# Kernel optimization log

Measured on AMD Instinct MI355X. Metric: run time of the kernel, lower is better.

## Reference

```python
import jax, jax.numpy as jnp
import numpy as np

HIDDEN_DIM = 256
Z_DIM = 64
B = 8
SRC_LEN = 2048
NUM_DIRS = 2


def setup_inputs() -> dict:
    key = jax.random.key(0)
    ks = jax.random.split(key, 7)
    return {
        "encoder_hidden_state": jax.random.normal(ks[0], (NUM_DIRS, B, HIDDEN_DIM), dtype=jnp.float32),
        "decoder_hidden_state": jax.random.normal(ks[1], (B, HIDDEN_DIM), dtype=jnp.float32),
        "latent_z_seq": jax.random.normal(ks[2], (B, SRC_LEN, Z_DIM), dtype=jnp.float32),
        "mask": jax.random.randint(ks[3], (B, SRC_LEN), 0, 2, dtype=jnp.int32),
        "weight_q": jax.random.normal(ks[4], (HIDDEN_DIM + Z_DIM, HIDDEN_DIM), dtype=jnp.float32),
        "weight_k": jax.random.normal(ks[5], (HIDDEN_DIM + Z_DIM, HIDDEN_DIM), dtype=jnp.float32),
        "weight_v": jax.random.normal(ks[6], (HIDDEN_DIM + Z_DIM, HIDDEN_DIM), dtype=jnp.float32),
    }


def reference(encoder_hidden_state, decoder_hidden_state, latent_z_seq, mask,
              weight_q, weight_k, weight_v):
    # decoder_hidden_state is accepted but unused (as in the original forward).
    src_len = latent_z_seq.shape[1]
    temperature = jnp.asarray(HIDDEN_DIM ** 0.5, latent_z_seq.dtype)
    # sum over directions/layers: [D,B,H] -> [B,H], broadcast along seq
    enc = jnp.sum(encoder_hidden_state, axis=0)  # [B,H]
    enc = jnp.broadcast_to(enc[:, None, :], (enc.shape[0], src_len, enc.shape[1]))
    attn_input = jnp.concatenate((enc, latent_z_seq), axis=2)  # [B,S,H+Z]
    q = jnp.einsum('bsd,dh->bsh', attn_input, weight_q)
    k = jnp.einsum('bsd,dh->bsh', attn_input, weight_k)
    v = jnp.einsum('bsd,dh->bsh', attn_input, weight_v)
    scores = jnp.einsum('bqh,bkh->bqk', q, k) / temperature  # [B,S,S]
    # mask[:, :, None] broadcasts along the key axis (masks query rows)
    scores = jnp.where(mask[:, :, None] == 0, jnp.asarray(-1e9, scores.dtype), scores)
    attn = jax.nn.softmax(scores, axis=-1)
    output = jnp.einsum('bqk,bkh->bqh', attn, v)  # [B,S,H]
    return (output, attn)
```

## Files before the change

### kernel.cpp

```cpp
#include <hip/hip_runtime.h>
#include <hip/hip_bf16.h>

#define B_ 8
#define S_ 2048
#define H_ 256
#define Z_ 64
#define CHK 32
#define NQCH 16
#define BS (B_*S_)
#define PSLD 40

typedef short bf16x8 __attribute__((ext_vector_type(8)));
typedef float f32x4 __attribute__((ext_vector_type(4)));

__device__ __forceinline__ unsigned short f2bf(float f) {
  __hip_bfloat16 h = __float2bfloat16(f);
  return *reinterpret_cast<unsigned short*>(&h);
}
__device__ __forceinline__ float bf2f(unsigned short u) {
  __hip_bfloat16 h;
  *reinterpret_cast<unsigned short*>(&h) = u;
  return __bfloat162float(h);
}

__device__ __forceinline__ void gl_lds16(const void* g, void* l) {
  __builtin_amdgcn_global_load_lds(
      (const __attribute__((address_space(1))) unsigned int*)(uintptr_t)g,
      (__attribute__((address_space(3))) unsigned int*)(uintptr_t)l,
      16, 0, 0);
}

__global__ __launch_bounds__(256) void k0_base(
    const float* __restrict__ enc, const float* __restrict__ Wq,
    const float* __restrict__ Wk, const float* __restrict__ Wv,
    float* __restrict__ q0, float* __restrict__ k0, float* __restrict__ v0) {
  int b = blockIdx.x;
  int h = threadIdx.x;
  __shared__ float encs[H_];
  encs[h] = enc[b*H_ + h] + enc[B_*H_ + b*H_ + h];
  __syncthreads();
  float aq = 0.f, ak = 0.f, av = 0.f;
  #pragma unroll 4
  for (int d = 0; d < H_; d++) {
    float e = encs[d];
    aq = fmaf(e, Wq[d*H_ + h], aq);
    ak = fmaf(e, Wk[d*H_ + h], ak);
    av = fmaf(e, Wv[d*H_ + h], av);
  }
  q0[b*H_ + h] = aq;
  k0[b*H_ + h] = ak;
  v0[b*H_ + h] = av;
}

__global__ __launch_bounds__(256) void k1_prep(
    const float* __restrict__ z, const float* __restrict__ Wq,
    const float* __restrict__ Wk, const float* __restrict__ Wv,
    const float* __restrict__ q0, const float* __restrict__ k0b, const float* __restrict__ v0,
    unsigned short* __restrict__ Qhi, unsigned short* __restrict__ Qlo,
    unsigned short* __restrict__ Khi, unsigned short* __restrict__ Klo,
    unsigned short* __restrict__ Vt) {
  int b  = blockIdx.x >> 7;
  int st = blockIdx.x & 127;
  int tid = threadIdx.x;
  __shared__ float zs[16*Z_];
  __shared__ float vbuf[16][H_];
  {
    const float4* zp = reinterpret_cast<const float4*>(z + ((size_t)b*S_ + st*16)*Z_);
    reinterpret_cast<float4*>(zs)[tid] = zp[tid];
  }
  __syncthreads();
  float bq = q0[b*H_ + tid], bk = k0b[b*H_ + tid], bv = v0[b*H_ + tid];
  float accq[16], acck[16], accv[16];
  #pragma unroll
  for (int s = 0; s < 16; s++) { accq[s] = bq; acck[s] = bk; accv[s] = bv; }
  #pragma unroll 2
  for (int z0 = 0; z0 < Z_; z0 += 8) {
    float wq[8], wk[8], wv[8];
    #pragma unroll
    for (int j = 0; j < 8; j++) {
      wq[j] = Wq[(H_+z0+j)*H_ + tid];
      wk[j] = Wk[(H_+z0+j)*H_ + tid];
      wv[j] = Wv[(H_+z0+j)*H_ + tid];
    }
    #pragma unroll
    for (int j = 0; j < 8; j++) {
      #pragma unroll
      for (int s = 0; s < 16; s++) {
        float zz = zs[s*Z_ + z0 + j];
        accq[s] = fmaf(zz, wq[j], accq[s]);
        acck[s] = fmaf(zz, wk[j], acck[s]);
        accv[s] = fmaf(zz, wv[j], accv[s]);
      }
    }
  }
  #pragma unroll
  for (int s = 0; s < 16; s++) {
    size_t row = ((size_t)b*S_ + st*16 + s)*H_ + tid;
    unsigned short qh = f2bf(accq[s]);
    Qhi[row] = qh;
    Qlo[row] = f2bf(accq[s] - bf2f(qh));
    unsigned short kh = f2bf(acck[s]);
    Khi[row] = kh;
    Klo[row] = f2bf(acck[s] - bf2f(kh));
    vbuf[s][tid] = accv[s];
  }
  __syncthreads();
  unsigned int pk[8];
  #pragma unroll
  for (int j = 0; j < 8; j++) {
    pk[j] = (unsigned int)f2bf(vbuf[2*j][tid]) |
            ((unsigned int)f2bf(vbuf[2*j+1][tid]) << 16);
  }
  uint4* vt4 = reinterpret_cast<uint4*>(Vt + ((size_t)b*H_ + tid)*S_ + st*16);
  vt4[0] = make_uint4(pk[0], pk[1], pk[2], pk[3]);
  vt4[1] = make_uint4(pk[4], pk[5], pk[6], pk[7]);
}

__global__ __launch_bounds__(256, 1) void k2_flash(
    const unsigned short* __restrict__ Qhi, const unsigned short* __restrict__ Qlo,
    const unsigned short* __restrict__ Khi, const unsigned short* __restrict__ Klo,
    const unsigned short* __restrict__ Vt, const int* __restrict__ mask,
    float* __restrict__ attn, float* __restrict__ Mq,
    unsigned short* __restrict__ Opart) {
  int bb    = blockIdx.x;
  int b     = bb & 7;
  int strip = (bb >> 3) & 15;
  int kq    = bb >> 7;
  int qb    = strip*128;
  int k0q   = kq*512;
  int tid  = threadIdx.x;
  int wave = tid >> 6;
  int lane = tid & 63;
  int l15  = lane & 15;
  int quad = lane >> 4;
  int qw   = qb + wave*32;

  __shared__ __align__(16) unsigned short KhiL[2][32*256];
  __shared__ __align__(16) unsigned short KloL[2][32*256];
  __shared__ __align__(16) unsigned short VtL[2][256*32];
  __shared__ __align__(16) unsigned short Ps[4][2][16*PSLD];

  const unsigned short* KhiB = Khi + (size_t)b*S_*H_;
  const unsigned short* KloB = Klo + (size_t)b*S_*H_;
  const unsigned short* VtB  = Vt  + (size_t)b*H_*S_;

  int sub = lane >> 5;
  int c5  = lane & 31;
  int hl  = lane >> 2;
  int jj  = lane & 3;

  auto dma_chunk = [&](int c) {
    int buf = c & 1;
    int kc = k0q + c*CHK;
    #pragma unroll
    for (int t = 0; t < 4; t++) {
      int i = wave*4 + t;
      int row = i*2 + sub;
      size_t gs = (size_t)(kc + row)*H_ + ((c5 ^ row)*8);
      gl_lds16(KhiB + gs, &KhiL[buf][i*512]);
      gl_lds16(KloB + gs, &KloL[buf][i*512]);
    }
    #pragma unroll
    for (int t = 0; t < 4; t++) {
      int i = wave*4 + t;
      int h = i*16 + hl;
      gl_lds16(VtB + (size_t)h*S_ + kc + ((jj ^ (hl & 3))*8), &VtL[buf][i*512]);
    }
  };

  bf16x8 qh[2][8], ql[2][8];
  #pragma unroll
  for (int qt = 0; qt < 2; qt++) {
    const unsigned short* qhp = Qhi + ((size_t)b*S_ + qw + qt*16 + l15)*H_ + quad*8;
    const unsigned short* qlp = Qlo + ((size_t)b*S_ + qw + qt*16 + l15)*H_ + quad*8;
    #pragma unroll
    for (int dc = 0; dc < 8; dc++) {
      qh[qt][dc] = *reinterpret_cast<const bf16x8*>(qhp + dc*32);
      ql[qt][dc] = *reinterpret_cast<const bf16x8*>(qlp + dc*32);
    }
  }
  int mrow[2][4];
  #pragma unroll
  for (int qt = 0; qt < 2; qt++)
    #pragma unroll
    for (int r = 0; r < 4; r++) mrow[qt][r] = mask[b*S_ + qw + qt*16 + quad*4 + r];

  f32x4 acc_o[2][16];
  #pragma unroll
  for (int qt = 0; qt < 2; qt++)
    #pragma unroll
    for (int ht = 0; ht < 16; ht++) acc_o[qt][ht] = (f32x4){0.f, 0.f, 0.f, 0.f};
  float m_run[2][4] = {{-1e30f,-1e30f,-1e30f,-1e30f},{-1e30f,-1e30f,-1e30f,-1e30f}};

  dma_chunk(0);
  __syncthreads();

  for (int c = 0; c < NQCH; c++) {
    if (c+1 < NQCH) dma_chunk(c+1);
    int buf = c & 1;
    int kc  = k0q + c*CHK;
    f32x4 sacc[2][2];
    #pragma unroll
    for (int kt = 0; kt < 2; kt++) {
      int row = kt*16 + l15;
      const unsigned short* khb = &KhiL[buf][row*256];
      const unsigned short* klb = &KloL[buf][row*256];
      f32x4 a0[2], a1[2];
      #pragma unroll
      for (int qt = 0; qt < 2; qt++) {
        a0[qt] = (f32x4){0.f,0.f,0.f,0.f};
        a1[qt] = (f32x4){0.f,0.f,0.f,0.f};
      }
      #pragma unroll
      for (int dc = 0; dc < 8; dc += 2) {
        int s0 = ((dc*4 + quad) ^ row) * 8;
        int s1 = (((dc+1)*4 + quad) ^ row) * 8;
        bf16x8 kh0 = *reinterpret_cast<const bf16x8*>(khb + s0);
        bf16x8 kl0 = *reinterpret_cast<const bf16x8*>(klb + s0);
        bf16x8 kh1 = *reinterpret_cast<const bf16x8*>(khb + s1);
        bf16x8 kl1 = *reinterpret_cast<const bf16x8*>(klb + s1);
        #pragma unroll
        for (int qt = 0; qt < 2; qt++) {
          a0[qt] = __builtin_amdgcn_mfma_f32_16x16x32_bf16(qh[qt][dc],   kh0, a0[qt], 0, 0, 0);
          a1[qt] = __builtin_amdgcn_mfma_f32_16x16x32_bf16(qh[qt][dc+1], kh1, a1[qt], 0, 0, 0);
          a0[qt] = __builtin_amdgcn_mfma_f32_16x16x32_bf16(ql[qt][dc],   kh0, a0[qt], 0, 0, 0);
          a1[qt] = __builtin_amdgcn_mfma_f32_16x16x32_bf16(ql[qt][dc+1], kh1, a1[qt], 0, 0, 0);
          a0[qt] = __builtin_amdgcn_mfma_f32_16x16x32_bf16(qh[qt][dc],   kl0, a0[qt], 0, 0, 0);
          a1[qt] = __builtin_amdgcn_mfma_f32_16x16x32_bf16(qh[qt][dc+1], kl1, a1[qt], 0, 0, 0);
        }
      }
      #pragma unroll
      for (int qt = 0; qt < 2; qt++) sacc[qt][kt] = a0[qt] + a1[qt];
    }
    float p[2][2][4], alpha[2][4];
    bool resc = false;
    #pragma unroll
    for (int qt = 0; qt < 2; qt++) {
      #pragma unroll
      for (int r = 0; r < 4; r++) {
        float se0 = mrow[qt][r] ? sacc[qt][0][r]*0.0625f : -1e9f;
        float se1 = mrow[qt][r] ? sacc[qt][1][r]*0.0625f : -1e9f;
        float ml = fmaxf(se0, se1);
        ml = fmaxf(ml, __shfl_xor(ml, 1));
        ml = fmaxf(ml, __shfl_xor(ml, 2));
        ml = fmaxf(ml, __shfl_xor(ml, 4));
        ml = fmaxf(ml, __shfl_xor(ml, 8));
        float mnew = fmaxf(m_run[qt][r], ml);
        alpha[qt][r] = __expf(m_run[qt][r] - mnew);
        p[qt][0][r] = __expf(se0 - mnew);
        p[qt][1][r] = __expf(se1 - mnew);
        m_run[qt][r] = mnew;
        resc |= (alpha[qt][r] < 1.f);
        attn[((size_t)b*S_ + qw + qt*16 + quad*4 + r)*S_ + kc + l15]      = se0;
        attn[((size_t)b*S_ + qw + qt*16 + quad*4 + r)*S_ + kc + 16 + l15] = se1;
      }
    }
    if (__any(resc)) {
      #pragma unroll
      for (int qt = 0; qt < 2; qt++)
        #pragma unroll
        for (int ht = 0; ht < 16; ht++) {
          acc_o[qt][ht][0] *= alpha[qt][0];
          acc_o[qt][ht][1] *= alpha[qt][1];
          acc_o[qt][ht][2] *= alpha[qt][2];
          acc_o[qt][ht][3] *= alpha[qt][3];
        }
    }
    #pragma unroll
    for (int qt = 0; qt < 2; qt++)
      #pragma unroll
      for (int kt = 0; kt < 2; kt++)
        #pragma unroll
        for (int r = 0; r < 4; r++)
          Ps[wave][qt][(quad*4 + r)*PSLD + kt*16 + l15] = f2bf(p[qt][kt][r]);
    bf16x8 pa0 = *reinterpret_cast<const bf16x8*>(&Ps[wave][0][l15*PSLD + quad*8]);
    bf16x8 pa1 = *reinterpret_cast<const bf16x8*>(&Ps[wave][1][l15*PSLD + quad*8]);
    #pragma unroll
    for (int ht = 0; ht < 16; ht++) {
      bf16x8 v = *reinterpret_cast<const bf16x8*>(
          &VtL[buf][(ht*16 + l15)*32 + ((quad ^ (l15 & 3))*8)]);
      acc_o[0][ht] = __builtin_amdgcn_mfma_f32_16x16x32_bf16(pa0, v, acc_o[0][ht], 0, 0, 0);
      acc_o[1][ht] = __builtin_amdgcn_mfma_f32_16x16x32_bf16(pa1, v, acc_o[1][ht], 0, 0, 0);
    }
    __syncthreads();
  }

  if (l15 == 0) {
    #pragma unroll
    for (int qt = 0; qt < 2; qt++)
      #pragma unroll
      for (int r = 0; r < 4; r++)
        Mq[kq*BS + b*S_ + qw + qt*16 + quad*4 + r] = m_run[qt][r];
  }
  #pragma unroll
  for (int qt = 0; qt < 2; qt++)
    #pragma unroll
    for (int ht = 0; ht < 16; ht++)
      #pragma unroll
      for (int r = 0; r < 4; r++) {
        size_t idx = ((size_t)kq*BS + b*S_ + qw + qt*16 + quad*4 + r)*H_ + ht*16 + l15;
        Opart[idx] = f2bf(acc_o[qt][ht][r]);
      }
}

__global__ __launch_bounds__(256) void k3_combine(
    const float* __restrict__ Mq, const unsigned short* __restrict__ Opart,
    float* __restrict__ attn, float* __restrict__ outp) {
  int gr  = blockIdx.x;
  int tid = threadIdx.x;
  int lane = tid & 63, wv = tid >> 6;
  __shared__ float red[4];
  float m0 = Mq[gr], m1 = Mq[BS + gr], m2 = Mq[2*BS + gr], m3 = Mq[3*BS + gr];
  float m = fmaxf(fmaxf(m0, m1), fmaxf(m2, m3));
  float4* pa = reinterpret_cast<float4*>(attn + (size_t)gr*S_ + tid*8);
  float4 x0 = pa[0], x1 = pa[1];
  x0.x = __expf(x0.x - m); x0.y = __expf(x0.y - m);
  x0.z = __expf(x0.z - m); x0.w = __expf(x0.w - m);
  x1.x = __expf(x1.x - m); x1.y = __expf(x1.y - m);
  x1.z = __expf(x1.z - m); x1.w = __expf(x1.w - m);
  float ps = x0.x + x0.y + x0.z + x0.w + x1.x + x1.y + x1.z + x1.w;
  ps += __shfl_xor(ps, 1);  ps += __shfl_xor(ps, 2);
  ps += __shfl_xor(ps, 4);  ps += __shfl_xor(ps, 8);
  ps += __shfl_xor(ps, 16); ps += __shfl_xor(ps, 32);
  if (lane == 0) red[wv] = ps;
  __syncthreads();
  float il = 1.f / (red[0] + red[1] + red[2] + red[3]);
  x0.x *= il; x0.y *= il; x0.z *= il; x0.w *= il;
  x1.x *= il; x1.y *= il; x1.z *= il; x1.w *= il;
  pa[0] = x0; pa[1] = x1;
  float o = __expf(m0 - m)*bf2f(Opart[(size_t)gr*H_ + tid])
          + __expf(m1 - m)*bf2f(Opart[((size_t)BS + gr)*H_ + tid])
          + __expf(m2 - m)*bf2f(Opart[((size_t)2*BS + gr)*H_ + tid])
          + __expf(m3 - m)*bf2f(Opart[((size_t)3*BS + gr)*H_ + tid]);
  outp[(size_t)gr*H_ + tid] = o * il;
}

extern "C" void kernel_launch(void* const* d_in, const int* in_sizes, int n_in,
                              void* d_out, int out_size, void* d_ws, size_t ws_size,
                              hipStream_t stream) {
  const float* enc = (const float*)d_in[0];
  const float* z   = (const float*)d_in[2];
  const int* mask  = (const int*)d_in[3];
  const float* Wq  = (const float*)d_in[4];
  const float* Wk  = (const float*)d_in[5];
  const float* Wv  = (const float*)d_in[6];

  char* ws = (char*)d_ws;
  const size_t MB = 1024*1024;
  unsigned short* Qhi = (unsigned short*)(ws);
  unsigned short* Qlo = (unsigned short*)(ws +  8*MB);
  unsigned short* Khi = (unsigned short*)(ws + 16*MB);
  unsigned short* Klo = (unsigned short*)(ws + 24*MB);
  unsigned short* Vt  = (unsigned short*)(ws + 32*MB);
  float* q0 = (float*)(ws + 40*MB);
  float* k0 = q0 + B_*H_;
  float* v0 = k0 + B_*H_;
  float* Mq = (float*)(ws + 41*MB);
  unsigned short* Opart = (unsigned short*)(ws + 42*MB);

  float* outp = (float*)d_out;
  float* attn = outp + (size_t)B_*S_*H_;

  k0_base<<<B_, 256, 0, stream>>>(enc, Wq, Wk, Wv, q0, k0, v0);
  k1_prep<<<B_*(S_/16), 256, 0, stream>>>(z, Wq, Wk, Wv, q0, k0, v0,
                                          Qhi, Qlo, Khi, Klo, Vt);
  k2_flash<<<B_*(S_/128)*4, 256, 0, stream>>>(Qhi, Qlo, Khi, Klo, Vt, mask,
                                              attn, Mq, Opart);
  k3_combine<<<B_*S_, 256, 0, stream>>>(Mq, Opart, attn, outp);
}
```

Before: 385.1 us.

## Split flash kernel into QK-only pass and separate PV pass from stored scores

The flash kernel now computes only QK scores, writes raw scaled scores to attn, and tracks the per-row max without online rescaling or PV accumulation. That frees V LDS buffers and accumulator registers, so the launch bound now allows 2 blocks per CU. A new kernel reads the stored scores back, exponentiates them against the global max, and does the PV MFMA with V streamed through LDS, also producing row sums. The final kernel just normalizes attn. This adds a full extra read of the 128MB attn matrix in exchange for higher occupancy and simpler inner loops. The LDS swizzles are also changed.

```diff
diff --git a/kernel.cpp b/kernel.cpp
--- a/kernel.cpp
+++ b/kernel.cpp
@@ -8,7 +8,6 @@
 #define CHK 32
 #define NQCH 16
 #define BS (B_*S_)
-#define PSLD 40
 
 typedef short bf16x8 __attribute__((ext_vector_type(8)));
 typedef float f32x4 __attribute__((ext_vector_type(4)));
@@ -21,6 +20,9 @@
   __hip_bfloat16 h;
   *reinterpret_cast<unsigned short*>(&h) = u;
   return __bfloat162float(h);
+}
+__device__ __forceinline__ unsigned int pack2(float a, float b) {
+  return (unsigned int)f2bf(a) | ((unsigned int)f2bf(b) << 16);
 }
 
 __device__ __forceinline__ void gl_lds16(const void* g, void* l) {
@@ -107,21 +109,18 @@
   __syncthreads();
   unsigned int pk[8];
   #pragma unroll
-  for (int j = 0; j < 8; j++) {
-    pk[j] = (unsigned int)f2bf(vbuf[2*j][tid]) |
-            ((unsigned int)f2bf(vbuf[2*j+1][tid]) << 16);
-  }
+  for (int j = 0; j < 8; j++)
+    pk[j] = pack2(vbuf[2*j][tid], vbuf[2*j+1][tid]);
   uint4* vt4 = reinterpret_cast<uint4*>(Vt + ((size_t)b*H_ + tid)*S_ + st*16);
   vt4[0] = make_uint4(pk[0], pk[1], pk[2], pk[3]);
   vt4[1] = make_uint4(pk[4], pk[5], pk[6], pk[7]);
 }
 
-__global__ __launch_bounds__(256, 1) void k2_flash(
+__global__ __launch_bounds__(256, 2) void k2_flash(
     const unsigned short* __restrict__ Qhi, const unsigned short* __restrict__ Qlo,
     const unsigned short* __restrict__ Khi, const unsigned short* __restrict__ Klo,
-    const unsigned short* __restrict__ Vt, const int* __restrict__ mask,
-    float* __restrict__ attn, float* __restrict__ Mq,
-    unsigned short* __restrict__ Opart) {
+    const int* __restrict__ mask,
+    float* __restrict__ attn, float* __restrict__ Mq) {
   int bb    = blockIdx.x;
   int b     = bb & 7;
   int strip = (bb >> 3) & 15;
@@ -137,17 +136,12 @@
 
   __shared__ __align__(16) unsigned short KhiL[2][32*256];
   __shared__ __align__(16) unsigned short KloL[2][32*256];
-  __shared__ __align__(16) unsigned short VtL[2][256*32];
-  __shared__ __align__(16) unsigned short Ps[4][2][16*PSLD];
 
   const unsigned short* KhiB = Khi + (size_t)b*S_*H_;
   const unsigned short* KloB = Klo + (size_t)b*S_*H_;
-  const unsigned short* VtB  = Vt  + (size_t)b*H_*S_;
 
   int sub = lane >> 5;
   int c5  = lane & 31;
-  int hl  = lane >> 2;
-  int jj  = lane & 3;
 
   auto dma_chunk = [&](int c) {
     int buf = c & 1;
@@ -156,15 +150,10 @@
     for (int t = 0; t < 4; t++) {
       int i = wave*4 + t;
       int row = i*2 + sub;
-      size_t gs = (size_t)(kc + row)*H_ + ((c5 ^ row)*8);
+      int lslot = c5 ^ ((row & 15) << 1);
+      size_t gs = (size_t)(kc + row)*H_ + lslot*8;
       gl_lds16(KhiB + gs, &KhiL[buf][i*512]);
       gl_lds16(KloB + gs, &KloL[buf][i*512]);
-    }
-    #pragma unroll
-    for (int t = 0; t < 4; t++) {
-      int i = wave*4 + t;
-      int h = i*16 + hl;
-      gl_lds16(VtB + (size_t)h*S_ + kc + ((jj ^ (hl & 3))*8), &VtL[buf][i*512]);
     }
   };
 
@@ -185,11 +174,6 @@
     #pragma unroll
     for (int r = 0; r < 4; r++) mrow[qt][r] = mask[b*S_ + qw + qt*16 + quad*4 + r];
 
-  f32x4 acc_o[2][16];
-  #pragma unroll
-  for (int qt = 0; qt < 2; qt++)
-    #pragma unroll
-    for (int ht = 0; ht < 16; ht++) acc_o[qt][ht] = (f32x4){0.f, 0.f, 0.f, 0.f};
   float m_run[2][4] = {{-1e30f,-1e30f,-1e30f,-1e30f},{-1e30f,-1e30f,-1e30f,-1e30f}};
 
   dma_chunk(0);
@@ -203,6 +187,7 @@
     #pragma unroll
     for (int kt = 0; kt < 2; kt++) {
       int row = kt*16 + l15;
+      int sw  = (row & 15) << 1;
       const unsigned short* khb = &KhiL[buf][row*256];
       const unsigned short* klb = &KloL[buf][row*256];
       f32x4 a0[2], a1[2];
@@ -213,8 +198,8 @@
       }
       #pragma unroll
       for (int dc = 0; dc < 8; dc += 2) {
-        int s0 = ((dc*4 + quad) ^ row) * 8;
-        int s1 = (((dc+1)*4 + quad) ^ row) * 8;
+        int s0 = ((dc*4 + quad) ^ sw) * 8;
+        int s1 = (((dc+1)*4 + quad) ^ sw) * 8;
         bf16x8 kh0 = *reinterpret_cast<const bf16x8*>(khb + s0);
         bf16x8 kl0 = *reinterpret_cast<const bf16x8*>(klb + s0);
         bf16x8 kh1 = *reinterpret_cast<const bf16x8*>(khb + s1);
@@ -232,107 +217,154 @@
       #pragma unroll
       for (int qt = 0; qt < 2; qt++) sacc[qt][kt] = a0[qt] + a1[qt];
     }
-    float p[2][2][4], alpha[2][4];
-    bool resc = false;
     #pragma unroll
     for (int qt = 0; qt < 2; qt++) {
       #pragma unroll
       for (int r = 0; r < 4; r++) {
         float se0 = mrow[qt][r] ? sacc[qt][0][r]*0.0625f : -1e9f;
         float se1 = mrow[qt][r] ? sacc[qt][1][r]*0.0625f : -1e9f;
-        float ml = fmaxf(se0, se1);
-        ml = fmaxf(ml, __shfl_xor(ml, 1));
-        ml = fmaxf(ml, __shfl_xor(ml, 2));
-        ml = fmaxf(ml, __shfl_xor(ml, 4));
-        ml = fmaxf(ml, __shfl_xor(ml, 8));
-        float mnew = fmaxf(m_run[qt][r], ml);
-        alpha[qt][r] = __expf(m_run[qt][r] - mnew);
-        p[qt][0][r] = __expf(se0 - mnew);
-        p[qt][1][r] = __expf(se1 - mnew);
-        m_run[qt][r] = mnew;
-        resc |= (alpha[qt][r] < 1.f);
-        attn[((size_t)b*S_ + qw + qt*16 + quad*4 + r)*S_ + kc + l15]      = se0;
-        attn[((size_t)b*S_ + qw + qt*16 + quad*4 + r)*S_ + kc + 16 + l15] = se1;
+        m_run[qt][r] = fmaxf(m_run[qt][r], fmaxf(se0, se1));
+        size_t rb = ((size_t)b*S_ + qw + qt*16 + quad*4 + r)*S_ + kc;
+        attn[rb + l15]      = se0;
+        attn[rb + 16 + l15] = se1;
       }
     }
-    if (__any(resc)) {
-      #pragma unroll
-      for (int qt = 0; qt < 2; qt++)
-        #pragma unroll
-        for (int ht = 0; ht < 16; ht++) {
-          acc_o[qt][ht][0] *= alpha[qt][0];
-          acc_o[qt][ht][1] *= alpha[qt][1];
-          acc_o[qt][ht][2] *= alpha[qt][2];
-          acc_o[qt][ht][3] *= alpha[qt][3];
-        }
-    }
-    #pragma unroll
-    for (int qt = 0; qt < 2; qt++)
-      #pragma unroll
-      for (int kt = 0; kt < 2; kt++)
-        #pragma unroll
-        for (int r = 0; r < 4; r++)
-          Ps[wave][qt][(quad*4 + r)*PSLD + kt*16 + l15] = f2bf(p[qt][kt][r]);
-    bf16x8 pa0 = *reinterpret_cast<const bf16x8*>(&Ps[wave][0][l15*PSLD + quad*8]);
-    bf16x8 pa1 = *reinterpret_cast<const bf16x8*>(&Ps[wave][1][l15*PSLD + quad*8]);
+    __syncthreads();
+  }
+
+  #pragma unroll
+  for (int qt = 0; qt < 2; qt++) {
+    #pragma unroll
+    for (int r = 0; r < 4; r++) {
+      float m = m_run[qt][r];
+      m = fmaxf(m, __shfl_xor(m, 1));
+      m = fmaxf(m, __shfl_xor(m, 2));
+      m = fmaxf(m, __shfl_xor(m, 4));
+      m = fmaxf(m, __shfl_xor(m, 8));
+      if (l15 == 0)
+        Mq[kq*BS + b*S_ + qw + qt*16 + quad*4 + r] = m;
+    }
+  }
+}
+
+__global__ __launch_bounds__(256) void k3a(
+    const float* __restrict__ attn, const unsigned short* __restrict__ Vt,
+    const float* __restrict__ Mq, float* __restrict__ outp,
+    float* __restrict__ Mfin, float* __restrict__ Lfin) {
+  int bb = blockIdx.x;
+  int b  = bb & 7;
+  int qb = (bb >> 3) * 64;
+  int tid  = threadIdx.x;
+  int wave = tid >> 6;
+  int lane = tid & 63;
+  int l15  = lane & 15;
+  int quad = lane >> 4;
+  int qw   = qb + wave*16;
+
+  __shared__ __align__(16) unsigned short VtL[2][256*64];
+  __shared__ float lred[4][16];
+
+  const unsigned short* VtB = Vt + (size_t)b*H_*S_;
+  int gr = b*S_ + qw + l15;
+  float m = fmaxf(fmaxf(Mq[gr], Mq[BS + gr]), fmaxf(Mq[2*BS + gr], Mq[3*BS + gr]));
+
+  int hsub = lane >> 3;
+  int slot = lane & 7;
+
+  auto dma_v = [&](int c) {
+    int buf = c & 1;
+    int kc = c*64;
+    #pragma unroll
+    for (int t = 0; t < 8; t++) {
+      int i = wave*8 + t;
+      int h = i*8 + hsub;
+      int lslot = slot ^ (((h >> 2) & 3) << 1);
+      gl_lds16(VtB + (size_t)h*S_ + kc + lslot*8, &VtL[buf][i*512]);
+    }
+  };
+
+  f32x4 acc[16];
+  #pragma unroll
+  for (int ht = 0; ht < 16; ht++) acc[ht] = (f32x4){0.f, 0.f, 0.f, 0.f};
+  float lpart = 0.f;
+
+  const float* sp = attn + (size_t)gr*S_ + quad*8;
+  dma_v(0);
+  float4 s0 = *reinterpret_cast<const float4*>(sp);
+  float4 s1 = *reinterpret_cast<const float4*>(sp + 4);
+  float4 s2 = *reinterpret_cast<const float4*>(sp + 32);
+  float4 s3 = *reinterpret_cast<const float4*>(sp + 36);
+  __syncthreads();
+
+  for (int c = 0; c < 32; c++) {
+    if (c+1 < 32) dma_v(c+1);
+    int buf = c & 1;
+    float4 n0, n1, n2, n3;
+    if (c+1 < 32) {
+      const float* np = sp + (c+1)*64;
+      n0 = *reinterpret_cast<const float4*>(np);
+      n1 = *reinterpret_cast<const float4*>(np + 4);
+      n2 = *reinterpret_cast<const float4*>(np + 32);
+      n3 = *reinterpret_cast<const float4*>(np + 36);
+    }
+    float p0 = __expf(s0.x - m), p1 = __expf(s0.y - m);
+    float p2 = __expf(s0.z - m), p3 = __expf(s0.w - m);
+    float p4 = __expf(s1.x - m), p5 = __expf(s1.y - m);
+    float p6 = __expf(s1.z - m), p7 = __expf(s1.w - m);
+    float q0f = __expf(s2.x - m), q1f = __expf(s2.y - m);
+    float q2f = __expf(s2.z - m), q3f = __expf(s2.w - m);
+    float q4f = __expf(s3.x - m), q5f = __expf(s3.y - m);
+    float q6f = __expf(s3.z - m), q7f = __expf(s3.w - m);
+    lpart += p0+p1+p2+p3+p4+p5+p6+p7+q0f+q1f+q2f+q3f+q4f+q5f+q6f+q7f;
+    unsigned int pw[4] = {pack2(p0,p1), pack2(p2,p3), pack2(p4,p5), pack2(p6,p7)};
+    unsigned int qv[4] = {pack2(q0f,q1f), pack2(q2f,q3f), pack2(q4f,q5f), pack2(q6f,q7f)};
+    bf16x8 pa0, pa1;
+    memcpy(&pa0, pw, 16);
+    memcpy(&pa1, qv, 16);
+    int swz = ((l15 >> 2) & 3) << 1;
     #pragma unroll
     for (int ht = 0; ht < 16; ht++) {
-      bf16x8 v = *reinterpret_cast<const bf16x8*>(
-          &VtL[buf][(ht*16 + l15)*32 + ((quad ^ (l15 & 3))*8)]);
-      acc_o[0][ht] = __builtin_amdgcn_mfma_f32_16x16x32_bf16(pa0, v, acc_o[0][ht], 0, 0, 0);
-      acc_o[1][ht] = __builtin_amdgcn_mfma_f32_16x16x32_bf16(pa1, v, acc_o[1][ht], 0, 0, 0);
-    }
+      const unsigned short* vb = &VtL[buf][(ht*16 + l15)*64];
+      bf16x8 v0 = *reinterpret_cast<const bf16x8*>(vb + (quad ^ swz)*8);
+      bf16x8 v1 = *reinterpret_cast<const bf16x8*>(vb + ((4 + quad) ^ swz)*8);
+      acc[ht] = __builtin_amdgcn_mfma_f32_16x16x32_bf16(pa0, v0, acc[ht], 0, 0, 0);
+      acc[ht] = __builtin_amdgcn_mfma_f32_16x16x32_bf16(pa1, v1, acc[ht], 0, 0, 0);
+    }
+    s0 = n0; s1 = n1; s2 = n2; s3 = n3;
     __syncthreads();
   }
 
-  if (l15 == 0) {
-    #pragma unroll
-    for (int qt = 0; qt < 2; qt++)
-      #pragma unroll
-      for (int r = 0; r < 4; r++)
-        Mq[kq*BS + b*S_ + qw + qt*16 + quad*4 + r] = m_run[qt][r];
-  }
-  #pragma unroll
-  for (int qt = 0; qt < 2; qt++)
-    #pragma unroll
-    for (int ht = 0; ht < 16; ht++)
-      #pragma unroll
-      for (int r = 0; r < 4; r++) {
-        size_t idx = ((size_t)kq*BS + b*S_ + qw + qt*16 + quad*4 + r)*H_ + ht*16 + l15;
-        Opart[idx] = f2bf(acc_o[qt][ht][r]);
-      }
-}
-
-__global__ __launch_bounds__(256) void k3_combine(
-    const float* __restrict__ Mq, const unsigned short* __restrict__ Opart,
-    float* __restrict__ attn, float* __restrict__ outp) {
+  lpart += __shfl_xor(lpart, 16);
+  lpart += __shfl_xor(lpart, 32);
+  if (quad == 0) {
+    lred[wave][l15] = lpart;
+    Lfin[gr] = lpart;
+    Mfin[gr] = m;
+  }
+  float il[4];
+  #pragma unroll
+  for (int r = 0; r < 4; r++) il[r] = 1.f / lred[wave][quad*4 + r];
+  #pragma unroll
+  for (int ht = 0; ht < 16; ht++)
+    #pragma unroll
+    for (int r = 0; r < 4; r++)
+      outp[((size_t)b*S_ + qw + quad*4 + r)*H_ + ht*16 + l15] = acc[ht][r] * il[r];
+}
+
+__global__ __launch_bounds__(256) void k3b(
+    float* __restrict__ attn, const float* __restrict__ Mfin,
+    const float* __restrict__ Lfin) {
   int gr  = blockIdx.x;
   int tid = threadIdx.x;
-  int lane = tid & 63, wv = tid >> 6;
-  __shared__ float red[4];
-  float m0 = Mq[gr], m1 = Mq[BS + gr], m2 = Mq[2*BS + gr], m3 = Mq[3*BS + gr];
-  float m = fmaxf(fmaxf(m0, m1), fmaxf(m2, m3));
+  float m  = Mfin[gr];
+  float il = 1.f / Lfin[gr];
   float4* pa = reinterpret_cast<float4*>(attn + (size_t)gr*S_ + tid*8);
   float4 x0 = pa[0], x1 = pa[1];
-  x0.x = __expf(x0.x - m); x0.y = __expf(x0.y - m);
-  x0.z = __expf(x0.z - m); x0.w = __expf(x0.w - m);
-  x1.x = __expf(x1.x - m); x1.y = __expf(x1.y - m);
-  x1.z = __expf(x1.z - m); x1.w = __expf(x1.w - m);
-  float ps = x0.x + x0.y + x0.z + x0.w + x1.x + x1.y + x1.z + x1.w;
-  ps += __shfl_xor(ps, 1);  ps += __shfl_xor(ps, 2);
-  ps += __shfl_xor(ps, 4);  ps += __shfl_xor(ps, 8);
-  ps += __shfl_xor(ps, 16); ps += __shfl_xor(ps, 32);
-  if (lane == 0) red[wv] = ps;
-  __syncthreads();
-  float il = 1.f / (red[0] + red[1] + red[2] + red[3]);
-  x0.x *= il; x0.y *= il; x0.z *= il; x0.w *= il;
-  x1.x *= il; x1.y *= il; x1.z *= il; x1.w *= il;
+  x0.x = __expf(x0.x - m)*il; x0.y = __expf(x0.y - m)*il;
+  x0.z = __expf(x0.z - m)*il; x0.w = __expf(x0.w - m)*il;
+  x1.x = __expf(x1.x - m)*il; x1.y = __expf(x1.y - m)*il;
+  x1.z = __expf(x1.z - m)*il; x1.w = __expf(x1.w - m)*il;
   pa[0] = x0; pa[1] = x1;
-  float o = __expf(m0 - m)*bf2f(Opart[(size_t)gr*H_ + tid])
-          + __expf(m1 - m)*bf2f(Opart[((size_t)BS + gr)*H_ + tid])
-          + __expf(m2 - m)*bf2f(Opart[((size_t)2*BS + gr)*H_ + tid])
-          + __expf(m3 - m)*bf2f(Opart[((size_t)3*BS + gr)*H_ + tid]);
-  outp[(size_t)gr*H_ + tid] = o * il;
 }
 
 extern "C" void kernel_launch(void* const* d_in, const int* in_sizes, int n_in,
@@ -355,8 +387,9 @@
   float* q0 = (float*)(ws + 40*MB);
   float* k0 = q0 + B_*H_;
   float* v0 = k0 + B_*H_;
-  float* Mq = (float*)(ws + 41*MB);
-  unsigned short* Opart = (unsigned short*)(ws + 42*MB);
+  float* Mq   = (float*)(ws + 41*MB);
+  float* Mfin = (float*)(ws + 41*MB + 512*1024);
+  float* Lfin = (float*)(ws + 41*MB + 512*1024 + 64*1024);
 
   float* outp = (float*)d_out;
   float* attn = outp + (size_t)B_*S_*H_;
@@ -364,7 +397,8 @@
   k0_base<<<B_, 256, 0, stream>>>(enc, Wq, Wk, Wv, q0, k0, v0);
   k1_prep<<<B_*(S_/16), 256, 0, stream>>>(z, Wq, Wk, Wv, q0, k0, v0,
                                           Qhi, Qlo, Khi, Klo, Vt);
-  k2_flash<<<B_*(S_/128)*4, 256, 0, stream>>>(Qhi, Qlo, Khi, Klo, Vt, mask,
-                                              attn, Mq, Opart);
-  k3_combine<<<B_*S_, 256, 0, stream>>>(Mq, Opart, attn, outp);
-}
+  k2_flash<<<B_*(S_/128)*4, 256, 0, stream>>>(Qhi, Qlo, Khi, Klo, mask,
+                                              attn, Mq);
+  k3a<<<B_*(S_/64), 256, 0, stream>>>(attn, Vt, Mq, outp, Mfin, Lfin);
+  k3b<<<B_*S_, 256, 0, stream>>>(attn, Mfin, Lfin);
+}
```

Result: faster. 338.0 us (-12.2%).
